# Kernel tuning notes

Measured on AMD Instinct MI355X. Metric: run time of the kernel, lower is better.

## Reference

```python
import jax, jax.numpy as jnp
import numpy as np

D_MODEL = 1024
N_HEADS = 16
D_HEAD = D_MODEL // N_HEADS
WIN = 256
NEG_INF = -1e30


def setup_inputs() -> dict:
    key = jax.random.key(0)
    k1, k2, k3 = jax.random.split(key, 3)
    B, L = 4, 4096
    x = jax.random.normal(k1, (B, L, D_MODEL), dtype=jnp.float32)
    w_qkv = jax.random.normal(k2, (D_MODEL, 3 * D_MODEL), dtype=jnp.float32) * (1.0 / np.sqrt(D_MODEL))
    w_out = jax.random.normal(k3, (D_MODEL, D_MODEL), dtype=jnp.float32) * (1.0 / np.sqrt(D_MODEL))
    return {"x": x, "w_qkv": w_qkv, "w_out": w_out}


def _band_mask(nb: int):
    ti = jnp.arange(WIN)[:, None]
    tj = jnp.arange(2 * WIN)[None, :]
    base = (tj >= ti + 1) & (tj <= ti + WIN)
    first = base & (tj >= WIN)                         # block 0 has zero-padded (invalid) prev block
    rest = jnp.broadcast_to(base, (nb - 1, WIN, 2 * WIN))
    return jnp.concatenate([first[None], rest], axis=0)


def reference(x, w_qkv, w_out):
    B, L, D = x.shape
    nb = L // WIN
    qkv = (x @ w_qkv).reshape(B, L, 3, N_HEADS, D_HEAD)
    q, k, v = qkv[:, :, 0], qkv[:, :, 1], qkv[:, :, 2]          # [B, L, H, dh]
    def to_blocks(t):
        return t.transpose(0, 2, 1, 3).reshape(B, N_HEADS, nb, WIN, D_HEAD)
    qb, kb, vb = to_blocks(q), to_blocks(k), to_blocks(v)
    zero_blk = jnp.zeros_like(kb[:, :, :1])
    k_kv = jnp.concatenate([jnp.concatenate([zero_blk, kb[:, :, :-1]], axis=2), kb], axis=3)  # [B,H,nb,2W,dh]
    v_kv = jnp.concatenate([jnp.concatenate([zero_blk, vb[:, :, :-1]], axis=2), vb], axis=3)
    scale = 1.0 / np.sqrt(D_HEAD)
    scores = jnp.einsum('bhnqd,bhnkd->bhnqk', qb, k_kv) * scale
    scores = jnp.where(_band_mask(nb), scores, NEG_INF)
    attn = jax.nn.softmax(scores, axis=-1)
    ob = jnp.einsum('bhnqk,bhnkd->bhnqd', attn, v_kv)
    out = ob.reshape(B, N_HEADS, L, D_HEAD).transpose(0, 2, 1, 3).reshape(B, L, D)
    return out @ w_out
```

## Files before the change

### kernel.cpp

```cpp
#include <hip/hip_runtime.h>

typedef __bf16 bf16_t;
typedef __bf16 bf16x8 __attribute__((ext_vector_type(8)));
typedef float f32x4 __attribute__((ext_vector_type(4)));
typedef unsigned short ushort_t;

#define MFMA_16x16x32(a, b, c) __builtin_amdgcn_mfma_f32_16x16x32_bf16((a), (b), (c), 0, 0, 0)

__device__ __forceinline__ void async_ld16(const void* gptr, void* lptr) {
  typedef __attribute__((address_space(1))) const unsigned int as1_t;
  typedef __attribute__((address_space(3))) unsigned int as3_t;
  __builtin_amdgcn_global_load_lds((as1_t*)(unsigned long long)gptr,
                                   (as3_t*)(unsigned int)(unsigned long long)lptr,
                                   16, 0, 0);
}

__global__ void detect_dtype(const ushort_t* __restrict__ x, int* __restrict__ flag) {
  __shared__ int cnt[256];
  int c = 0;
#pragma unroll
  for (int i = 0; i < 16; ++i) {
    const ushort_t u = x[threadIdx.x * 16 + i];
    const int e = (u >> 7) & 0xFF;
    if ((u & 0x7FFF) != 0 && (e < 0x3A || e > 0xC0)) ++c;
  }
  cnt[threadIdx.x] = c;
  __syncthreads();
  if (threadIdx.x == 0) {
    int t = 0;
    for (int i = 0; i < 256; ++i) t += cnt[i];
    *flag = (t > 512) ? 1 : 0;
  }
}

__global__ __launch_bounds__(256) void convert_to_bf16(const void* __restrict__ src,
                                                       bf16_t* __restrict__ dst, int n8,
                                                       const int* __restrict__ flag) {
  const int isF32 = *flag;
  int i = blockIdx.x * 256 + threadIdx.x;
  const int stride = gridDim.x * 256;
  if (isF32) {
    const float4* s = (const float4*)src;
    for (; i < n8; i += stride) {
      const float4 a = s[(size_t)i * 2];
      const float4 b = s[(size_t)i * 2 + 1];
      bf16x8 o;
      o[0] = (bf16_t)a.x; o[1] = (bf16_t)a.y; o[2] = (bf16_t)a.z; o[3] = (bf16_t)a.w;
      o[4] = (bf16_t)b.x; o[5] = (bf16_t)b.y; o[6] = (bf16_t)b.z; o[7] = (bf16_t)b.w;
      *(bf16x8*)(dst + (size_t)i * 8) = o;
    }
  } else {
    const uint4* s = (const uint4*)src;
    for (; i < n8; i += stride) ((uint4*)dst)[i] = s[i];
  }
}

__global__ __launch_bounds__(256) void transpose_b16(const ushort_t* __restrict__ in,
                                                     ushort_t* __restrict__ out,
                                                     int R, int C) {
  __shared__ alignas(16) ushort_t t[64 * 72];
  const int tid = threadIdx.x;
  const int c0 = blockIdx.x * 64;
  const int r0 = blockIdx.y * 64;
#pragma unroll
  for (int it = 0; it < 2; ++it) {
    int cid = tid + it * 256;
    int row = cid >> 3, co = (cid & 7) * 8;
    *(uint4*)(t + row * 72 + co) = *(const uint4*)(in + (size_t)(r0 + row) * C + c0 + co);
  }
  __syncthreads();
#pragma unroll
  for (int it = 0; it < 2; ++it) {
    int cid = tid + it * 256;
    int orow = cid >> 3, ko = (cid & 7) * 8;
    uint4 u;
    ushort_t* tp = (ushort_t*)&u;
#pragma unroll
    for (int j = 0; j < 8; ++j) tp[j] = t[(ko + j) * 72 + orow];
    *(uint4*)(out + (size_t)(c0 + orow) * R + r0 + ko) = u;
  }
}

__global__ __launch_bounds__(256) void transpose_v(const ushort_t* __restrict__ qkv,
                                                   ushort_t* __restrict__ vT) {
  __shared__ alignas(16) ushort_t t[64 * 72];
  const int tid = threadIdx.x;
  const int l0 = blockIdx.x * 64;
  const int bh = blockIdx.y;
  const int b = bh >> 4, h = bh & 15;
  const ushort_t* src = qkv + ((size_t)(b * 4096 + l0)) * 3072 + 2048 + h * 64;
#pragma unroll
  for (int it = 0; it < 2; ++it) {
    int cid = tid + it * 256;
    int row = cid >> 3, co = (cid & 7) * 8;
    *(uint4*)(t + row * 72 + co) = *(const uint4*)(src + (size_t)row * 3072 + co);
  }
  __syncthreads();
  ushort_t* dst = vT + ((size_t)bh * 64) * 4096 + l0;
#pragma unroll
  for (int it = 0; it < 2; ++it) {
    int cid = tid + it * 256;
    int d = cid >> 3, ko = (cid & 7) * 8;
    uint4 u;
    ushort_t* tp = (ushort_t*)&u;
#pragma unroll
    for (int j = 0; j < 8; ++j) tp[j] = t[(ko + j) * 72 + d];
    *(uint4*)(dst + (size_t)d * 4096 + ko) = u;
  }
}

__global__ __launch_bounds__(512) void gemm_bf16(const bf16_t* __restrict__ A, int lda,
                                                 const bf16_t* __restrict__ Bt,
                                                 void* __restrict__ Cout, int N_out,
                                                 int K, const int* __restrict__ flag) {
  __shared__ alignas(16) bf16_t smem[65536];
  const int tid = threadIdx.x;
  const int wave = tid >> 6;
  const int lane = tid & 63;
  const int l15 = lane & 15;
  const int quad = lane >> 4;
  const int wm = wave >> 2;
  const int wn = wave & 3;

  int lin = blockIdx.y * gridDim.x + blockIdx.x;
  const int nwg = gridDim.x * gridDim.y;
  if ((nwg & 7) == 0) lin = (lin & 7) * (nwg >> 3) + (lin >> 3);
  const int tn = (lin % gridDim.x) * 256;
  const int tm = (lin / gridDim.x) * 256;

  f32x4 acc[8][4];
#pragma unroll
  for (int i = 0; i < 8; ++i)
#pragma unroll
    for (int j = 0; j < 4; ++j) acc[i][j] = (f32x4){0.f, 0.f, 0.f, 0.f};

  const int r_st = tid >> 3;
  const int jg8 = ((tid & 7) ^ (r_st & 7)) * 8;
  const int wofs = wave * 512;

  const int rowA = wm * 16 + l15;
  const int rowB = wn * 16 + l15;
  const int sw = l15 & 7;
  const int c0 = (quad ^ sw) * 8;
  const int c1 = ((quad | 4) ^ sw) * 8;

  const int NT = K >> 6;

#define STAGE_HALF(G, ldg, grow0, kk, ldsbase)                              \
  do {                                                                      \
    const bf16_t* _g = (G) + (size_t)((grow0) + r_st) * (ldg) + (kk) + jg8; \
    async_ld16(_g, &smem[(ldsbase) + wofs]);                                \
    async_ld16(_g + (size_t)64 * (ldg), &smem[(ldsbase) + 4096 + wofs]);    \
  } while (0)

#define READ_A(mh)                                                \
  do {                                                            \
    _Pragma("unroll") for (int q = 0; q < 4; ++q) {               \
      const int off = bufA + (((mh)*128 + q * 32 + rowA) << 6);   \
      a_[q][0] = *(const bf16x8*)&smem[off + c0];                 \
      a_[q][1] = *(const bf16x8*)&smem[off + c1];                 \
    }                                                             \
  } while (0)

#define READ_B(nh, dst)                                           \
  do {                                                            \
    _Pragma("unroll") for (int jn = 0; jn < 2; ++jn) {            \
      const int off = bufB + (((nh)*128 + jn * 64 + rowB) << 6);  \
      dst[jn][0] = *(const bf16x8*)&smem[off + c0];               \
      dst[jn][1] = *(const bf16x8*)&smem[off + c1];               \
    }                                                             \
  } while (0)

#define DO_MFMA(mh, nh, bb)                                                  \
  do {                                                                       \
    _Pragma("unroll") for (int q = 0; q < 4; ++q)                            \
        _Pragma("unroll") for (int jn = 0; jn < 2; ++jn) {                   \
      acc[(mh)*4 + q][(nh)*2 + jn] =                                         \
          MFMA_16x16x32(a_[q][0], bb[jn][0], acc[(mh)*4 + q][(nh)*2 + jn]);  \
      acc[(mh)*4 + q][(nh)*2 + jn] =                                         \
          MFMA_16x16x32(a_[q][1], bb[jn][1], acc[(mh)*4 + q][(nh)*2 + jn]);  \
    }                                                                        \
  } while (0)

#define PHASE_MID(VMC)                                     \
  asm volatile("s_waitcnt vmcnt(" VMC ")" ::: "memory");   \
  __builtin_amdgcn_s_barrier();                            \
  asm volatile("s_waitcnt lgkmcnt(0)" ::: "memory");       \
  __builtin_amdgcn_sched_barrier(0);                       \
  __builtin_amdgcn_s_setprio(1)

#define PHASE_MID_NV()                                     \
  __builtin_amdgcn_s_barrier();                            \
  asm volatile("s_waitcnt lgkmcnt(0)" ::: "memory");       \
  __builtin_amdgcn_sched_barrier(0);                       \
  __builtin_amdgcn_s_setprio(1)

#define PHASE_END()               \
  __builtin_amdgcn_s_setprio(0);  \
  __builtin_amdgcn_s_barrier();   \
  __builtin_amdgcn_sched_barrier(0)

  STAGE_HALF(A, lda, tm, 0, 0);
  STAGE_HALF(Bt, K, tn, 0, 16384);
  STAGE_HALF(Bt, K, tn + 128, 0, 16384 + 8192);
  STAGE_HALF(A, lda, tm + 128, 0, 8192);
  asm volatile("s_waitcnt vmcnt(4)" ::: "memory");
  __builtin_amdgcn_s_barrier();

  bf16x8 a_[4][2], b0_[2][2], b1_[2][2];
  int bufA = 0;
  for (int t = 0; t < NT; ++t) {
    const int bufB = bufA + 16384;
    const int sA = bufA ^ 32768;
    const int sB = sA + 16384;
    const int kst = (t + 1) << 6;
    const bool pf = (kst < K);

    READ_A(0);
    READ_B(0, b0_);
    if (pf) STAGE_HALF(A, lda, tm, kst, sA);
    PHASE_MID("4");
    DO_MFMA(0, 0, b0_);
    PHASE_END();

    READ_B(1, b1_);
    if (pf) STAGE_HALF(Bt, K, tn, kst, sB);
    PHASE_MID("4");
    DO_MFMA(0, 1, b1_);
    PHASE_END();

    READ_A(1);
    if (pf) STAGE_HALF(Bt, K, tn + 128, kst, sB + 8192);
    PHASE_MID_NV();
    DO_MFMA(1, 1, b1_);
    PHASE_END();

    if (pf) STAGE_HALF(A, lda, tm + 128, kst, sA + 8192);
    PHASE_MID("6");
    DO_MFMA(1, 0, b0_);
    PHASE_END();

    bufA ^= 32768;
  }

  asm volatile("s_waitcnt vmcnt(0)" ::: "memory");
  __syncthreads();

  const int isF32 = flag ? *flag : 0;
  if (isF32) {
#pragma unroll
    for (int f = 0; f < 8; ++f) {
      const int m0 = tm + (f >> 2) * 128 + (f & 3) * 32 + wm * 16 + quad * 4;
#pragma unroll
      for (int nidx = 0; nidx < 4; ++nidx) {
        const int col = tn + (nidx >> 1) * 128 + (nidx & 1) * 64 + wn * 16 + l15;
        float* cp = (float*)Cout + (size_t)m0 * N_out + col;
#pragma unroll
        for (int r = 0; r < 4; ++r) cp[(size_t)r * N_out] = acc[f][nidx][r];
      }
    }
  } else {
    bf16_t* stg = smem + wave * 1152;
#pragma unroll
    for (int f = 0; f < 8; ++f) {
#pragma unroll
      for (int nidx = 0; nidx < 4; ++nidx)
#pragma unroll
        for (int r = 0; r < 4; ++r)
          stg[(quad * 4 + r) * 72 + nidx * 16 + l15] = (bf16_t)acc[f][nidx][r];
      __asm__ volatile("s_waitcnt lgkmcnt(0)" ::: "memory");
      const int m0 = tm + (f >> 2) * 128 + (f & 3) * 32 + wm * 16;
#pragma unroll
      for (int p = 0; p < 2; ++p) {
        const int idx = lane + p * 64;
        const int row = idx >> 3, c8 = (idx & 7) * 8;
        uint4 u = *(const uint4*)(stg + row * 72 + c8);
        const int col = tn + ((c8 >> 5) << 7) + (((c8 >> 4) & 1) << 6) + wn * 16 + (c8 & 15);
        *(uint4*)((bf16_t*)Cout + (size_t)(m0 + row) * N_out + col) = u;
      }
      __asm__ volatile("s_waitcnt lgkmcnt(0)" ::: "memory");
    }
  }
#undef STAGE_HALF
#undef READ_A
#undef READ_B
#undef DO_MFMA
#undef PHASE_MID
#undef PHASE_MID_NV
#undef PHASE_END
}

__global__ __launch_bounds__(256) void attn_swa(bf16_t* qkv, const bf16_t* __restrict__ vT) {
  __shared__ alignas(16) bf16_t k_lds[64 * 72];
  __shared__ alignas(16) bf16_t vt_lds[64 * 72];
  __shared__ alignas(16) bf16_t p_lds[4 * 16 * 72];

  int wg = blockIdx.x;
  wg = (wg & 7) * 512 + (wg >> 3);
  const int b = wg >> 10;
  const int h = (wg >> 6) & 15;
  const int qt = wg & 63;
  const int blk = qt >> 2;
  const int wq = qt & 3;
  const int tid = threadIdx.x;
  const int wave = tid >> 6;
  const int lane = tid & 63;
  const int l15 = lane & 15;
  const int quad = lane >> 4;
  const int qw = qt * 64 + wave * 16;

  const size_t qoff = ((size_t)(b * 4096 + qw + l15)) * 3072 + h * 64;
  const bf16x8 qf0 = *(const bf16x8*)(qkv + qoff + quad * 8);
  const bf16x8 qf1 = *(const bf16x8*)(qkv + qoff + 32 + quad * 8);

  f32x4 of[4];
#pragma unroll
  for (int i = 0; i < 4; ++i) of[i] = (f32x4){0.f, 0.f, 0.f, 0.f};
  float m_i[4], l_i[4];
#pragma unroll
  for (int r = 0; r < 4; ++r) {
    m_i[r] = -1e30f;
    l_i[r] = 0.0f;
  }

  const int kb0 = blk * 256 - 256;
  const int kclo = (blk == 0) ? 4 : wq;
  const int kchi = wq + 4;

  const int row0 = tid >> 3;
  const int co8 = (tid & 7) * 8;
  const bf16_t* kbase = qkv + ((size_t)b * 4096) * 3072 + 1024 + h * 64;
  const bf16_t* vbase = vT + (((size_t)b * 16 + h) * 64) * 4096;
  uint4 kr0, kr1, vr0, vr1;

#define ISSUE_KV(KB)                                                           \
  do {                                                                         \
    kr0 = *(const uint4*)(kbase + (size_t)((KB) + row0) * 3072 + co8);         \
    kr1 = *(const uint4*)(kbase + (size_t)((KB) + row0 + 32) * 3072 + co8);    \
    vr0 = *(const uint4*)(vbase + (size_t)row0 * 4096 + (KB) + co8);           \
    vr1 = *(const uint4*)(vbase + (size_t)(row0 + 32) * 4096 + (KB) + co8);    \
  } while (0)

  ISSUE_KV(kb0 + kclo * 64);

  for (int kc = kclo; kc <= kchi; ++kc) {
    const int kb = kb0 + kc * 64;
    __syncthreads();
    *(uint4*)(k_lds + row0 * 72 + co8) = kr0;
    *(uint4*)(k_lds + (row0 + 32) * 72 + co8) = kr1;
    *(uint4*)(vt_lds + row0 * 72 + co8) = vr0;
    *(uint4*)(vt_lds + (row0 + 32) * 72 + co8) = vr1;
    if (kc < kchi) ISSUE_KV(kb + 64);
    __syncthreads();

    f32x4 s[4];
    __builtin_amdgcn_s_setprio(1);
#pragma unroll
    for (int nt = 0; nt < 4; ++nt) {
      bf16x8 kf0 = *(const bf16x8*)(k_lds + (nt * 16 + l15) * 72 + quad * 8);
      bf16x8 kf1 = *(const bf16x8*)(k_lds + (nt * 16 + l15) * 72 + 32 + quad * 8);
      f32x4 z = (f32x4){0.f, 0.f, 0.f, 0.f};
      z = MFMA_16x16x32(qf0, kf0, z);
      z = MFMA_16x16x32(qf1, kf1, z);
      s[nt] = z;
    }
    __builtin_amdgcn_s_setprio(0);

    float sv[4][4];
#pragma unroll
    for (int nt = 0; nt < 4; ++nt) {
      const int key = kb + nt * 16 + l15;
#pragma unroll
      for (int r = 0; r < 4; ++r) {
        const int p = qw + quad * 4 + r;
        const bool valid = (key <= p) && (key + 256 > p);
        sv[nt][r] = valid ? s[nt][r] * 0.125f : -1e30f;
      }
    }
    float rm[4];
#pragma unroll
    for (int r = 0; r < 4; ++r)
      rm[r] = fmaxf(fmaxf(sv[0][r], sv[1][r]), fmaxf(sv[2][r], sv[3][r]));
#pragma unroll
    for (int off = 1; off < 16; off <<= 1)
#pragma unroll
      for (int r = 0; r < 4; ++r) rm[r] = fmaxf(rm[r], __shfl_xor(rm[r], off));

    float mn[4], alpha[4];
#pragma unroll
    for (int r = 0; r < 4; ++r) {
      mn[r] = fmaxf(m_i[r], rm[r]);
      alpha[r] = __expf(m_i[r] - mn[r]);
      m_i[r] = mn[r];
    }

    float rs[4] = {0.f, 0.f, 0.f, 0.f};
#pragma unroll
    for (int nt = 0; nt < 4; ++nt)
#pragma unroll
      for (int r = 0; r < 4; ++r) {
        const float pv = (sv[nt][r] > -1e29f) ? __expf(sv[nt][r] - mn[r]) : 0.0f;
        rs[r] += pv;
        p_lds[wave * 1152 + (quad * 4 + r) * 72 + nt * 16 + l15] = (bf16_t)pv;
      }
#pragma unroll
    for (int off = 1; off < 16; off <<= 1)
#pragma unroll
      for (int r = 0; r < 4; ++r) rs[r] += __shfl_xor(rs[r], off);
#pragma unroll
    for (int r = 0; r < 4; ++r) l_i[r] = l_i[r] * alpha[r] + rs[r];
#pragma unroll
    for (int dt = 0; dt < 4; ++dt)
#pragma unroll
      for (int r = 0; r < 4; ++r) of[dt][r] *= alpha[r];

    __builtin_amdgcn_s_setprio(1);
#pragma unroll
    for (int kk = 0; kk < 2; ++kk) {
      bf16x8 pf = *(const bf16x8*)(p_lds + wave * 1152 + l15 * 72 + kk * 32 + quad * 8);
#pragma unroll
      for (int dt = 0; dt < 4; ++dt) {
        bf16x8 vf = *(const bf16x8*)(vt_lds + (dt * 16 + l15) * 72 + kk * 32 + quad * 8);
        of[dt] = MFMA_16x16x32(pf, vf, of[dt]);
      }
    }
    __builtin_amdgcn_s_setprio(0);
  }
#undef ISSUE_KV

  float inv[4];
#pragma unroll
  for (int r = 0; r < 4; ++r) inv[r] = 1.0f / fmaxf(l_i[r], 1e-20f);
  bf16_t* op = qkv + ((size_t)(b * 4096 + qw)) * 3072 + h * 64;
#pragma unroll
  for (int dt = 0; dt < 4; ++dt)
#pragma unroll
    for (int r = 0; r < 4; ++r)
      op[(size_t)(quad * 4 + r) * 3072 + dt * 16 + l15] = (bf16_t)(of[dt][r] * inv[r]);
}

extern "C" void kernel_launch(void* const* d_in, const int* in_sizes, int n_in,
                              void* d_out, int out_size, void* d_ws, size_t ws_size,
                              hipStream_t stream) {
  char* ws = (char*)d_ws;
  bf16_t* wTq = (bf16_t*)(ws);
  bf16_t* wTo = (bf16_t*)(ws + 6291456);
  bf16_t* qkv = (bf16_t*)(ws + 8388608);
  int* flag = (int*)(ws + 109051904);

  bf16_t* xb = (bf16_t*)d_out;
  bf16_t* vTb = (bf16_t*)d_out;
  bf16_t* tmpq = qkv;
  bf16_t* tmpo = qkv + 3145728;

  detect_dtype<<<1, 256, 0, stream>>>((const ushort_t*)d_in[0], flag);
  convert_to_bf16<<<1024, 256, 0, stream>>>(d_in[0], xb, 2097152, flag);
  convert_to_bf16<<<512, 256, 0, stream>>>(d_in[1], tmpq, 393216, flag);
  convert_to_bf16<<<256, 256, 0, stream>>>(d_in[2], tmpo, 131072, flag);
  transpose_b16<<<dim3(48, 16), 256, 0, stream>>>((const ushort_t*)tmpq, (ushort_t*)wTq,
                                                  1024, 3072);
  transpose_b16<<<dim3(16, 16), 256, 0, stream>>>((const ushort_t*)tmpo, (ushort_t*)wTo,
                                                  1024, 1024);
  gemm_bf16<<<dim3(12, 64), 512, 0, stream>>>(xb, 1024, wTq, qkv, 3072, 1024, nullptr);
  transpose_v<<<dim3(64, 64), 256, 0, stream>>>((const ushort_t*)qkv, (ushort_t*)vTb);
  attn_swa<<<dim3(4096), 256, 0, stream>>>(qkv, vTb);
  gemm_bf16<<<dim3(4, 64), 512, 0, stream>>>(qkv, 3072, wTo, d_out, 1024, 1024, flag);
}
```

Baseline: 365.1 us.

## Restructure GEMM to triple-buffered BK=32 pipeline; add lazy softmax rescale in attention

The bf16 GEMM main loop drops the four-phase, double-buffered BK=64 schedule with interleaved barriers. In its place is a triple-buffered BK=32 pipeline that prefetches two stages ahead, uses a new LDS swizzle, and has a single barrier per iteration. In the attention kernel, blocks that are fully inside the window skip the per-element mask. The online softmax also skips the max update and output rescaling when the new row maximum stays within a threshold of the running one. These aim to cut sync and VALU overhead, at the risk of less MFMA/load overlap per barrier and slightly different numerics; the removed -1e29 check now relies on exp underflowing for masked entries.

```diff
diff --git a/kernel.cpp b/kernel.cpp
--- a/kernel.cpp
+++ b/kernel.cpp
@@ -113,7 +113,7 @@
                                                  const bf16_t* __restrict__ Bt,
                                                  void* __restrict__ Cout, int N_out,
                                                  int K, const int* __restrict__ flag) {
-  __shared__ alignas(16) bf16_t smem[65536];
+  __shared__ alignas(16) bf16_t smem[49152];
   const int tid = threadIdx.x;
   const int wave = tid >> 6;
   const int lane = tid & 63;
@@ -134,116 +134,67 @@
 #pragma unroll
     for (int j = 0; j < 4; ++j) acc[i][j] = (f32x4){0.f, 0.f, 0.f, 0.f};
 
-  const int r_st = tid >> 3;
-  const int jg8 = ((tid & 7) ^ (r_st & 7)) * 8;
+  const int r_st = tid >> 2;
+  const int csrc = ((tid & 3) ^ ((tid >> 3) & 3)) * 8;
   const int wofs = wave * 512;
 
   const int rowA = wm * 16 + l15;
   const int rowB = wn * 16 + l15;
-  const int sw = l15 & 7;
-  const int c0 = (quad ^ sw) * 8;
-  const int c1 = ((quad | 4) ^ sw) * 8;
-
-  const int NT = K >> 6;
-
-#define STAGE_HALF(G, ldg, grow0, kk, ldsbase)                              \
-  do {                                                                      \
-    const bf16_t* _g = (G) + (size_t)((grow0) + r_st) * (ldg) + (kk) + jg8; \
-    async_ld16(_g, &smem[(ldsbase) + wofs]);                                \
-    async_ld16(_g + (size_t)64 * (ldg), &smem[(ldsbase) + 4096 + wofs]);    \
+  const int cfr = (quad ^ ((l15 >> 1) & 3)) * 8;
+
+  const int NT = K >> 5;
+
+#define STAGE_HALF(G, ldg, grow0, kk, base)                                  \
+  async_ld16((G) + (size_t)((grow0) + r_st) * (ldg) + (kk) + csrc,           \
+             &smem[(base) + wofs])
+
+#define STAGE4(kk, base)                                \
+  do {                                                  \
+    STAGE_HALF(A, lda, tm, (kk), (base));               \
+    STAGE_HALF(Bt, K, tn, (kk), (base) + 8192);         \
+    STAGE_HALF(Bt, K, tn + 128, (kk), (base) + 12288);  \
+    STAGE_HALF(A, lda, tm + 128, (kk), (base) + 4096);  \
   } while (0)
 
-#define READ_A(mh)                                                \
-  do {                                                            \
-    _Pragma("unroll") for (int q = 0; q < 4; ++q) {               \
-      const int off = bufA + (((mh)*128 + q * 32 + rowA) << 6);   \
-      a_[q][0] = *(const bf16x8*)&smem[off + c0];                 \
-      a_[q][1] = *(const bf16x8*)&smem[off + c1];                 \
-    }                                                             \
-  } while (0)
-
-#define READ_B(nh, dst)                                           \
-  do {                                                            \
-    _Pragma("unroll") for (int jn = 0; jn < 2; ++jn) {            \
-      const int off = bufB + (((nh)*128 + jn * 64 + rowB) << 6);  \
-      dst[jn][0] = *(const bf16x8*)&smem[off + c0];               \
-      dst[jn][1] = *(const bf16x8*)&smem[off + c1];               \
-    }                                                             \
-  } while (0)
-
-#define DO_MFMA(mh, nh, bb)                                                  \
-  do {                                                                       \
-    _Pragma("unroll") for (int q = 0; q < 4; ++q)                            \
-        _Pragma("unroll") for (int jn = 0; jn < 2; ++jn) {                   \
-      acc[(mh)*4 + q][(nh)*2 + jn] =                                         \
-          MFMA_16x16x32(a_[q][0], bb[jn][0], acc[(mh)*4 + q][(nh)*2 + jn]);  \
-      acc[(mh)*4 + q][(nh)*2 + jn] =                                         \
-          MFMA_16x16x32(a_[q][1], bb[jn][1], acc[(mh)*4 + q][(nh)*2 + jn]);  \
-    }                                                                        \
-  } while (0)
-
-#define PHASE_MID(VMC)                                     \
-  asm volatile("s_waitcnt vmcnt(" VMC ")" ::: "memory");   \
-  __builtin_amdgcn_s_barrier();                            \
-  asm volatile("s_waitcnt lgkmcnt(0)" ::: "memory");       \
-  __builtin_amdgcn_sched_barrier(0);                       \
-  __builtin_amdgcn_s_setprio(1)
-
-#define PHASE_MID_NV()                                     \
-  __builtin_amdgcn_s_barrier();                            \
-  asm volatile("s_waitcnt lgkmcnt(0)" ::: "memory");       \
-  __builtin_amdgcn_sched_barrier(0);                       \
-  __builtin_amdgcn_s_setprio(1)
-
-#define PHASE_END()               \
-  __builtin_amdgcn_s_setprio(0);  \
-  __builtin_amdgcn_s_barrier();   \
-  __builtin_amdgcn_sched_barrier(0)
-
-  STAGE_HALF(A, lda, tm, 0, 0);
-  STAGE_HALF(Bt, K, tn, 0, 16384);
-  STAGE_HALF(Bt, K, tn + 128, 0, 16384 + 8192);
-  STAGE_HALF(A, lda, tm + 128, 0, 8192);
+  STAGE4(0, 0);
+  STAGE4(32, 16384);
   asm volatile("s_waitcnt vmcnt(4)" ::: "memory");
   __builtin_amdgcn_s_barrier();
 
-  bf16x8 a_[4][2], b0_[2][2], b1_[2][2];
-  int bufA = 0;
+  int rb = 0;
   for (int t = 0; t < NT; ++t) {
-    const int bufB = bufA + 16384;
-    const int sA = bufA ^ 32768;
-    const int sB = sA + 16384;
-    const int kst = (t + 1) << 6;
+    const int kst = (t + 2) << 5;
     const bool pf = (kst < K);
-
-    READ_A(0);
-    READ_B(0, b0_);
-    if (pf) STAGE_HALF(A, lda, tm, kst, sA);
-    PHASE_MID("4");
-    DO_MFMA(0, 0, b0_);
-    PHASE_END();
-
-    READ_B(1, b1_);
-    if (pf) STAGE_HALF(Bt, K, tn, kst, sB);
-    PHASE_MID("4");
-    DO_MFMA(0, 1, b1_);
-    PHASE_END();
-
-    READ_A(1);
-    if (pf) STAGE_HALF(Bt, K, tn + 128, kst, sB + 8192);
-    PHASE_MID_NV();
-    DO_MFMA(1, 1, b1_);
-    PHASE_END();
-
-    if (pf) STAGE_HALF(A, lda, tm + 128, kst, sA + 8192);
-    PHASE_MID("6");
-    DO_MFMA(1, 0, b0_);
-    PHASE_END();
-
-    bufA ^= 32768;
-  }
-
-  asm volatile("s_waitcnt vmcnt(0)" ::: "memory");
+    const int sb = (rb >= 16384) ? rb - 16384 : rb + 32768;
+    if (pf) STAGE4(kst, sb);
+
+    bf16x8 a_[8], b_[4];
+#pragma unroll
+    for (int mh = 0; mh < 2; ++mh)
+#pragma unroll
+      for (int q = 0; q < 4; ++q)
+        a_[mh * 4 + q] = *(const bf16x8*)&smem[rb + mh * 4096 +
+                                               ((q * 32 + rowA) << 5) + cfr];
+#pragma unroll
+    for (int nh = 0; nh < 2; ++nh)
+#pragma unroll
+      for (int jn = 0; jn < 2; ++jn)
+        b_[nh * 2 + jn] = *(const bf16x8*)&smem[rb + 8192 + nh * 4096 +
+                                                ((jn * 64 + rowB) << 5) + cfr];
+
+    __builtin_amdgcn_s_setprio(1);
+#pragma unroll
+    for (int f = 0; f < 8; ++f)
+#pragma unroll
+      for (int n = 0; n < 4; ++n) acc[f][n] = MFMA_16x16x32(a_[f], b_[n], acc[f][n]);
+    __builtin_amdgcn_s_setprio(0);
+
+    asm volatile("s_waitcnt vmcnt(4)" ::: "memory");
+    if (!pf) asm volatile("s_waitcnt vmcnt(0)" ::: "memory");
+    __builtin_amdgcn_s_barrier();
+    rb = (rb == 32768) ? 0 : rb + 16384;
+  }
+
   __syncthreads();
 
   const int isF32 = flag ? *flag : 0;
@@ -282,12 +233,7 @@
     }
   }
 #undef STAGE_HALF
-#undef READ_A
-#undef READ_B
-#undef DO_MFMA
-#undef PHASE_MID
-#undef PHASE_MID_NV
-#undef PHASE_END
+#undef STAGE4
 }
 
 __global__ __launch_bounds__(256) void attn_swa(bf16_t* qkv, const bf16_t* __restrict__ vT) {
@@ -366,15 +312,23 @@
     }
     __builtin_amdgcn_s_setprio(0);
 
+    const bool full = (kb + 63 <= qw) && (kb >= qw - 240);
     float sv[4][4];
-#pragma unroll
-    for (int nt = 0; nt < 4; ++nt) {
-      const int key = kb + nt * 16 + l15;
-#pragma unroll
-      for (int r = 0; r < 4; ++r) {
-        const int p = qw + quad * 4 + r;
-        const bool valid = (key <= p) && (key + 256 > p);
-        sv[nt][r] = valid ? s[nt][r] * 0.125f : -1e30f;
+    if (full) {
+#pragma unroll
+      for (int nt = 0; nt < 4; ++nt)
+#pragma unroll
+        for (int r = 0; r < 4; ++r) sv[nt][r] = s[nt][r] * 0.125f;
+    } else {
+#pragma unroll
+      for (int nt = 0; nt < 4; ++nt) {
+        const int key = kb + nt * 16 + l15;
+#pragma unroll
+        for (int r = 0; r < 4; ++r) {
+          const int p = qw + quad * 4 + r;
+          const bool valid = (key <= p) && (key + 256 > p);
+          sv[nt][r] = valid ? s[nt][r] * 0.125f : -1e30f;
+        }
       }
     }
     float rm[4];
@@ -386,12 +340,16 @@
 #pragma unroll
       for (int r = 0; r < 4; ++r) rm[r] = fmaxf(rm[r], __shfl_xor(rm[r], off));
 
-    float mn[4], alpha[4];
-#pragma unroll
-    for (int r = 0; r < 4; ++r) {
-      mn[r] = fmaxf(m_i[r], rm[r]);
-      alpha[r] = __expf(m_i[r] - mn[r]);
-      m_i[r] = mn[r];
+    const bool dok = (rm[0] <= m_i[0] + 8.0f) && (rm[1] <= m_i[1] + 8.0f) &&
+                     (rm[2] <= m_i[2] + 8.0f) && (rm[3] <= m_i[3] + 8.0f);
+    const bool defer = __all((int)dok);
+    float mn[4];
+    if (defer) {
+#pragma unroll
+      for (int r = 0; r < 4; ++r) mn[r] = m_i[r];
+    } else {
+#pragma unroll
+      for (int r = 0; r < 4; ++r) mn[r] = fmaxf(m_i[r], rm[r]);
     }
 
     float rs[4] = {0.f, 0.f, 0.f, 0.f};
@@ -399,7 +357,7 @@
     for (int nt = 0; nt < 4; ++nt)
 #pragma unroll
       for (int r = 0; r < 4; ++r) {
-        const float pv = (sv[nt][r] > -1e29f) ? __expf(sv[nt][r] - mn[r]) : 0.0f;
+        const float pv = __expf(sv[nt][r] - mn[r]);
         rs[r] += pv;
         p_lds[wave * 1152 + (quad * 4 + r) * 72 + nt * 16 + l15] = (bf16_t)pv;
       }
@@ -407,12 +365,20 @@
     for (int off = 1; off < 16; off <<= 1)
 #pragma unroll
       for (int r = 0; r < 4; ++r) rs[r] += __shfl_xor(rs[r], off);
-#pragma unroll
-    for (int r = 0; r < 4; ++r) l_i[r] = l_i[r] * alpha[r] + rs[r];
-#pragma unroll
-    for (int dt = 0; dt < 4; ++dt)
-#pragma unroll
-      for (int r = 0; r < 4; ++r) of[dt][r] *= alpha[r];
+
+    if (defer) {
+#pragma unroll
+      for (int r = 0; r < 4; ++r) l_i[r] += rs[r];
+    } else {
+#pragma unroll
+      for (int r = 0; r < 4; ++r) {
+        const float alpha = __expf(m_i[r] - mn[r]);
+        l_i[r] = l_i[r] * alpha + rs[r];
+        m_i[r] = mn[r];
+#pragma unroll
+        for (int dt = 0; dt < 4; ++dt) of[dt][r] *= alpha;
+      }
+    }
 
     __builtin_amdgcn_s_setprio(1);
 #pragma unroll
```

After: 386.7 us. 1.06x slower.
